# Kernel optimization log

Hardware: AMD Instinct MI355X
Metric: run time of the kernel (lower is better)

## Reference

```python
import jax, jax.numpy as jnp
import numpy as np

N = 100000   # nodes
E = 3200000  # edges (avg degree 32)
F = 128      # input node feature dim
C = 32       # GCSConv channels
H = 24       # dense1 units


def setup_inputs() -> dict:
    key = jax.random.key(0)
    ks = jax.random.split(key, 12)
    rng = np.random.default_rng(0)
    src = rng.integers(0, N, size=E, dtype=np.int32)
    dst = rng.integers(0, N, size=E, dtype=np.int32)
    # GCN-style symmetric normalization weights: D^{-1/2} A D^{-1/2}
    deg_out = np.maximum(np.bincount(src, minlength=N), 1).astype(np.float32)
    deg_in = np.maximum(np.bincount(dst, minlength=N), 1).astype(np.float32)
    w = 1.0 / np.sqrt(deg_out[src] * deg_in[dst])
    glorot = lambda k, fin, fout: jax.random.normal(k, (fin, fout), jnp.float32) * np.sqrt(2.0 / (fin + fout))
    return {
        "x": jax.random.normal(ks[0], (N, F), jnp.float32),
        "edge_src": jnp.asarray(src),
        "edge_dst": jnp.asarray(dst),
        "edge_w": jnp.asarray(w),
        "K1a": glorot(ks[1], F, C), "K2a": glorot(ks[2], F, C), "ba": jnp.zeros((C,), jnp.float32),
        "K1b": glorot(ks[3], C, C), "K2b": glorot(ks[4], C, C), "bb": jnp.zeros((C,), jnp.float32),
        "Wd1": glorot(ks[5], C, H), "bd1": jnp.zeros((H,), jnp.float32),
        "Wd2": glorot(ks[6], H, 1), "bd2": jnp.zeros((1,), jnp.float32),
    }


def _gcs_conv(x, src, dst, w, K1, K2, b):
    # Spektral GCSConv: relu(A_norm @ (x @ K1) + x @ K2 + b)
    h = x @ K1                                   # [N, C] transform first (cheap dim)
    msg = h[src] * w[:, None]                    # [E, C] gather + scale
    agg = jax.ops.segment_sum(msg, dst, num_segments=N)  # [N, C] scatter-add
    return jax.nn.relu(agg + x @ K2 + b)


def reference(x, edge_src, edge_dst, edge_w, K1a, K2a, ba, K1b, K2b, bb, Wd1, bd1, Wd2, bd2):
    x = _gcs_conv(x, edge_src, edge_dst, edge_w, K1a, K2a, ba)
    x = _gcs_conv(x, edge_src, edge_dst, edge_w, K1b, K2b, bb)
    pooled = jnp.sum(x, axis=0, keepdims=True)   # GlobalSumPool -> [1, C]
    out = pooled @ Wd1 + bd1                     # Dense(24), linear
    out = out @ Wd2 + bd2                        # Dense(1), linear
    return out
```

## Files before the change

kernel.cpp:

```cpp
#include <hip/hip_runtime.h>
#include <hip/hip_bf16.h>

typedef unsigned long long ull;
typedef unsigned int uint;
typedef unsigned short ushort;

using bf16x8 = __attribute__((ext_vector_type(8))) short;
using f32x4  = __attribute__((ext_vector_type(4))) float;


#define CHUNK    8192
#define NPB      256
#define NBMAX    512
#define STAGECAP 9216

__device__ __forceinline__ ushort f2bf(float f) {
    __hip_bfloat16 b = __float2bfloat16(f);
    return *reinterpret_cast<ushort*>(&b);
}
__device__ __forceinline__ uint pack2(float a, float b) {
    return (uint)f2bf(a) | ((uint)f2bf(b) << 16);
}
__device__ __forceinline__ void bf16x4_decode(uint2 hv, float& f0, float& f1,
                                              float& f2, float& f3) {
    f0 = __uint_as_float(hv.x << 16);
    f1 = __uint_as_float(hv.x & 0xFFFF0000u);
    f2 = __uint_as_float(hv.y << 16);
    f3 = __uint_as_float(hv.y & 0xFFFF0000u);
}

__global__ __launch_bounds__(256) void prep_weights(
    const float* __restrict__ K1a, const float* __restrict__ K2a,
    const float* __restrict__ K1b, const float* __restrict__ K2b,
    ushort* __restrict__ Kca, ushort* __restrict__ Kcb)
{
    int t = blockIdx.x * 256 + threadIdx.x;
    if (t < 8192) {
        int col = t >> 7, k = t & 127;
        float v = (col < 32) ? K1a[k * 32 + col] : K2a[k * 32 + col - 32];
        Kca[col * 128 + k] = f2bf(v);
    }
    if (t < 2048) {
        int col = t >> 5, k = t & 31;
        float v = (col < 32) ? K1b[k * 32 + col] : K2b[k * 32 + col - 32];
        Kcb[col * 32 + k] = f2bf(v);
    }
}

__global__ __launch_bounds__(512) void build_runs_kernel(
    const int* __restrict__ src, const int* __restrict__ dst,
    const float* __restrict__ w,
    ull* __restrict__ etmp, int* __restrict__ runoff,
    int* __restrict__ bucket_cnt, int e, int nruns, int nb)
{
    __shared__ ull stage[CHUNK];
    __shared__ int hist[NBMAX];
    __shared__ int scn[NBMAX];
    const int r = blockIdx.x, tid = threadIdx.x;
    const int base = r * CHUNK;
    const int cnt = min(CHUNK, e - base);

    hist[tid] = 0;
    __syncthreads();

    int dreg[CHUNK / 512];
    #pragma unroll
    for (int k = 0; k < CHUNK / 512; ++k) {
        int i = tid + k * 512;
        int d = (i < cnt) ? dst[base + i] : -1;
        dreg[k] = d;
        if (d >= 0) atomicAdd(&hist[d >> 8], 1);
    }
    __syncthreads();

    int v = hist[tid];
    scn[tid] = v;
    __syncthreads();
    for (int off = 1; off < NBMAX; off <<= 1) {
        int u = (tid >= off) ? scn[tid - off] : 0;
        __syncthreads();
        scn[tid] += u;
        __syncthreads();
    }
    const int ex = scn[tid] - v;
    if (tid < nb && v) atomicAdd(&bucket_cnt[tid], v);
    hist[tid] = ex;
    if (tid <= nb) runoff[(size_t)r * (nb + 1) + tid] = base + ex;
    __syncthreads();

    #pragma unroll
    for (int k = 0; k < CHUNK / 512; ++k) {
        int i = tid + k * 512;
        int d = dreg[k];
        if (d >= 0) {
            int pos = atomicAdd(&hist[d >> 8], 1);
            unsigned lo = (unsigned)src[base + i] | ((unsigned)(d & 255) << 20);
            stage[pos] = (ull)lo | ((ull)__float_as_uint(w[base + i]) << 32);
        }
    }
    __syncthreads();

    for (int i = tid; i < cnt; i += 512) etmp[base + i] = stage[i];
}

__global__ __launch_bounds__(512) void bucket_scan_kernel(
    const int* __restrict__ cnt, int* __restrict__ basep, int nb, int e)
{
    __shared__ int s[512];
    int t = threadIdx.x;
    int v = (t < nb) ? cnt[t] : 0;
    s[t] = v; __syncthreads();
    for (int off = 1; off < 512; off <<= 1) {
        int u = (t >= off) ? s[t - off] : 0;
        __syncthreads(); s[t] += u; __syncthreads();
    }
    if (t < nb) basep[t] = s[t] - v;
    if (t == 0) basep[nb] = e;
}

__global__ __launch_bounds__(512) void sort_buckets_kernel(
    const ull* __restrict__ etmp, const int* __restrict__ runoff,
    const int* __restrict__ bbase,
    ull* __restrict__ epack, int* __restrict__ row,
    int n, int e, int nruns, int nb)
{
    __shared__ ull stage[STAGECAP];
    __shared__ int hist[NPB];
    __shared__ int scn[NPB];
    __shared__ int cur[NPB];
    const int b = blockIdx.x, tid = threadIdx.x;
    const int base0 = bbase[b];
    const int cnt = bbase[b + 1] - base0;

    if (tid < NPB) hist[tid] = 0;
    __syncthreads();

    const int stream = tid >> 3, sub = tid & 7;
    const int* rs = runoff;

    for (int r = stream; r < nruns; r += 64) {
        int s0 = rs[(size_t)r * (nb + 1) + b];
        int s1 = rs[(size_t)r * (nb + 1) + b + 1];
        for (int i = s0 + sub; i < s1; i += 8)
            atomicAdd(&hist[(int)((etmp[i] >> 20) & 255u)], 1);
    }
    __syncthreads();

    int v = (tid < NPB) ? hist[tid] : 0;
    if (tid < NPB) scn[tid] = v;
    __syncthreads();
    for (int off = 1; off < NPB; off <<= 1) {
        int u = (tid >= off && tid < NPB) ? scn[tid - off] : 0;
        __syncthreads();
        if (tid < NPB) scn[tid] += u;
        __syncthreads();
    }
    if (tid < NPB) {
        int ex = scn[tid] - v;
        cur[tid] = ex;
        int node = b * NPB + tid;
        if (node < n) row[node] = base0 + ex;
    }
    if (b == nb - 1 && tid == 0) row[n] = e;
    __syncthreads();

    if (cnt <= STAGECAP) {
        for (int r = stream; r < nruns; r += 64) {
            int s0 = rs[(size_t)r * (nb + 1) + b];
            int s1 = rs[(size_t)r * (nb + 1) + b + 1];
            for (int i = s0 + sub; i < s1; i += 8) {
                ull pk = etmp[i];
                int pos = atomicAdd(&cur[(int)((pk >> 20) & 255u)], 1);
                stage[pos] = pk;
            }
        }
        __syncthreads();
        for (int i = tid; i < cnt; i += 512) epack[(size_t)base0 + i] = stage[i];
    } else {
        for (int r = stream; r < nruns; r += 64) {
            int s0 = rs[(size_t)r * (nb + 1) + b];
            int s1 = rs[(size_t)r * (nb + 1) + b + 1];
            for (int i = s0 + sub; i < s1; i += 8) {
                ull pk = etmp[i];
                int pos = atomicAdd(&cur[(int)((pk >> 20) & 255u)], 1);
                epack[(size_t)base0 + pos] = pk;
            }
        }
    }
}

__global__ __launch_bounds__(256) void gemm_mfma_a(
    const float* __restrict__ x, const ushort* __restrict__ Kca,
    const float* __restrict__ bias,
    ushort* __restrict__ h, float* __restrict__ p, int n)
{
    __shared__ ushort xs[64 * 136];
    const int tid = threadIdx.x;
    const int base = blockIdx.x * 64;

    for (int idx = tid; idx < 64 * 16; idx += 256) {
        int nl = idx >> 4, c8 = idx & 15;
        int node = base + nl;
        float4 v0 = make_float4(0.f, 0.f, 0.f, 0.f);
        float4 v1 = v0;
        if (node < n) {
            const float* xp = x + (size_t)node * 128 + c8 * 8;
            v0 = *(const float4*)xp;
            v1 = *(const float4*)(xp + 4);
        }
        uint4 u;
        u.x = pack2(v0.x, v0.y); u.y = pack2(v0.z, v0.w);
        u.z = pack2(v1.x, v1.y); u.w = pack2(v1.z, v1.w);
        *(uint4*)&xs[nl * 136 + c8 * 8] = u;
    }
    __syncthreads();

    const int lane = tid & 63, w = tid >> 6;
    const int r15 = lane & 15, g = lane >> 4;
    const int nbase = w * 16;

    f32x4 acc[4] = {{0.f,0.f,0.f,0.f},{0.f,0.f,0.f,0.f},
                    {0.f,0.f,0.f,0.f},{0.f,0.f,0.f,0.f}};

    #pragma unroll
    for (int kk = 0; kk < 4; ++kk) {
        bf16x8 af = *(const bf16x8*)&xs[(nbase + r15) * 136 + kk * 32 + g * 8];
        #pragma unroll
        for (int t = 0; t < 4; ++t) {
            bf16x8 bfr = *(const bf16x8*)&Kca[(size_t)(t * 16 + r15) * 128 + kk * 32 + g * 8];
            acc[t] = __builtin_amdgcn_mfma_f32_16x16x32_bf16(af, bfr, acc[t], 0, 0, 0);
        }
    }

    #pragma unroll
    for (int t = 0; t < 4; ++t) {
        int col = t * 16 + r15;
        float bv = (col >= 32) ? bias[col - 32] : 0.f;
        #pragma unroll
        for (int i = 0; i < 4; ++i) {
            int node = base + nbase + g * 4 + i;
            if (node < n) {
                float v = acc[t][i];
                if (col < 32) h[(size_t)node * 32 + col] = f2bf(v);
                else          p[(size_t)node * 32 + col - 32] = v + bv;
            }
        }
    }
}

__global__ __launch_bounds__(256) void gemm_mfma_b(
    const ushort* __restrict__ x1, const ushort* __restrict__ Kcb,
    const float* __restrict__ bias,
    ushort* __restrict__ h, float* __restrict__ p, int n)
{
    __shared__ ushort xs[64 * 40];
    const int tid = threadIdx.x;
    const int base = blockIdx.x * 64;

    {
        int nl = tid >> 2, c8 = tid & 3;
        int node = base + nl;
        uint4 u = make_uint4(0u, 0u, 0u, 0u);
        if (node < n) u = *(const uint4*)(x1 + (size_t)node * 32 + c8 * 8);
        *(uint4*)&xs[nl * 40 + c8 * 8] = u;
    }
    __syncthreads();

    const int lane = tid & 63, w = tid >> 6;
    const int r15 = lane & 15, g = lane >> 4;
    const int nbase = w * 16;

    f32x4 acc[4] = {{0.f,0.f,0.f,0.f},{0.f,0.f,0.f,0.f},
                    {0.f,0.f,0.f,0.f},{0.f,0.f,0.f,0.f}};

    bf16x8 af = *(const bf16x8*)&xs[(nbase + r15) * 40 + g * 8];
    #pragma unroll
    for (int t = 0; t < 4; ++t) {
        bf16x8 bfr = *(const bf16x8*)&Kcb[(size_t)(t * 16 + r15) * 32 + g * 8];
        acc[t] = __builtin_amdgcn_mfma_f32_16x16x32_bf16(af, bfr, acc[t], 0, 0, 0);
    }

    #pragma unroll
    for (int t = 0; t < 4; ++t) {
        int col = t * 16 + r15;
        float bv = (col >= 32) ? bias[col - 32] : 0.f;
        #pragma unroll
        for (int i = 0; i < 4; ++i) {
            int node = base + nbase + g * 4 + i;
            if (node < n) {
                float v = acc[t][i];
                if (col < 32) h[(size_t)node * 32 + col] = f2bf(v);
                else          p[(size_t)node * 32 + col - 32] = v + bv;
            }
        }
    }
}

__device__ __forceinline__ float4 gather_node(
    const int* __restrict__ row, const ull* __restrict__ epack,
    const ushort* __restrict__ h, int node, int q)
{
    int r0 = row[node], r1 = row[node + 1];
    float4 a = make_float4(0.f, 0.f, 0.f, 0.f);
    float4 b = make_float4(0.f, 0.f, 0.f, 0.f);
    int i = r0;
    for (; i + 7 < r1; i += 8) {
        ull pk[8];
        uint2 hv[8];
        #pragma unroll
        for (int u = 0; u < 8; ++u) pk[u] = epack[i + u];
        #pragma unroll
        for (int u = 0; u < 8; ++u)
            hv[u] = *(const uint2*)(h + (size_t)(pk[u] & 0xFFFFFu) * 32 + q * 4);
        #pragma unroll
        for (int u = 0; u < 8; ++u) {
            float wv = __uint_as_float((uint)(pk[u] >> 32));
            float f0, f1, f2, f3;
            bf16x4_decode(hv[u], f0, f1, f2, f3);
            if (u & 1) {
                b.x = fmaf(wv, f0, b.x); b.y = fmaf(wv, f1, b.y);
                b.z = fmaf(wv, f2, b.z); b.w = fmaf(wv, f3, b.w);
            } else {
                a.x = fmaf(wv, f0, a.x); a.y = fmaf(wv, f1, a.y);
                a.z = fmaf(wv, f2, a.z); a.w = fmaf(wv, f3, a.w);
            }
        }
    }
    for (; i + 3 < r1; i += 4) {
        ull pk[4];
        uint2 hv[4];
        #pragma unroll
        for (int u = 0; u < 4; ++u) pk[u] = epack[i + u];
        #pragma unroll
        for (int u = 0; u < 4; ++u)
            hv[u] = *(const uint2*)(h + (size_t)(pk[u] & 0xFFFFFu) * 32 + q * 4);
        #pragma unroll
        for (int u = 0; u < 4; ++u) {
            float wv = __uint_as_float((uint)(pk[u] >> 32));
            float f0, f1, f2, f3;
            bf16x4_decode(hv[u], f0, f1, f2, f3);
            if (u & 1) {
                b.x = fmaf(wv, f0, b.x); b.y = fmaf(wv, f1, b.y);
                b.z = fmaf(wv, f2, b.z); b.w = fmaf(wv, f3, b.w);
            } else {
                a.x = fmaf(wv, f0, a.x); a.y = fmaf(wv, f1, a.y);
                a.z = fmaf(wv, f2, a.z); a.w = fmaf(wv, f3, a.w);
            }
        }
    }
    for (; i < r1; ++i) {
        ull p0 = epack[i];
        uint2 h0 = *(const uint2*)(h + (size_t)(p0 & 0xFFFFFu) * 32 + q * 4);
        float w0 = __uint_as_float((uint)(p0 >> 32));
        float f0, f1, f2, f3;
        bf16x4_decode(h0, f0, f1, f2, f3);
        a.x = fmaf(w0, f0, a.x); a.y = fmaf(w0, f1, a.y);
        a.z = fmaf(w0, f2, a.z); a.w = fmaf(w0, f3, a.w);
    }
    a.x += b.x; a.y += b.y; a.z += b.z; a.w += b.w;
    return a;
}

__global__ __launch_bounds__(256) void gather_x1_kernel(
    const int* __restrict__ row, const ull* __restrict__ epack,
    const ushort* __restrict__ h, const float* __restrict__ p,
    ushort* __restrict__ x1, int n)
{
    const int q = threadIdx.x & 7;
    const int node = blockIdx.x * 32 + (threadIdx.x >> 3);
    if (node >= n) return;
    float4 acc = gather_node(row, epack, h, node, q);
    const float4 pv = *(const float4*)(p + (size_t)node * 32 + q * 4);
    float4 o;
    o.x = fmaxf(acc.x + pv.x, 0.f);
    o.y = fmaxf(acc.y + pv.y, 0.f);
    o.z = fmaxf(acc.z + pv.z, 0.f);
    o.w = fmaxf(acc.w + pv.w, 0.f);
    uint2 u;
    u.x = pack2(o.x, o.y);
    u.y = pack2(o.z, o.w);
    *(uint2*)(x1 + (size_t)node * 32 + q * 4) = u;
}

__global__ __launch_bounds__(256) void gather_pool_kernel(
    const int* __restrict__ row, const ull* __restrict__ epack,
    const ushort* __restrict__ h, const float* __restrict__ p,
    float* __restrict__ pooled, int n)
{
    const int q = threadIdx.x & 7;
    const int node = blockIdx.x * 32 + (threadIdx.x >> 3);

    float4 o = make_float4(0.f, 0.f, 0.f, 0.f);
    if (node < n) {
        float4 acc = gather_node(row, epack, h, node, q);
        const float4 pv = *(const float4*)(p + (size_t)node * 32 + q * 4);
        o.x = fmaxf(acc.x + pv.x, 0.f);
        o.y = fmaxf(acc.y + pv.y, 0.f);
        o.z = fmaxf(acc.z + pv.z, 0.f);
        o.w = fmaxf(acc.w + pv.w, 0.f);
    }
    __shared__ float red[256][4];
    red[threadIdx.x][0] = o.x; red[threadIdx.x][1] = o.y;
    red[threadIdx.x][2] = o.z; red[threadIdx.x][3] = o.w;
    __syncthreads();
    if (threadIdx.x < 32) {
        const int c = threadIdx.x;
        const int cq = c >> 2, cj = c & 3;
        float s = 0.f;
        #pragma unroll
        for (int l = 0; l < 32; ++l) s += red[l * 8 + cq][cj];
        unsafeAtomicAdd(&pooled[c], s);
    }
}

__device__ __forceinline__ void store_row_bf16(ushort* out, const float* acc) {
    uint u[16];
    #pragma unroll
    for (int k = 0; k < 16; ++k) u[k] = pack2(acc[2 * k], acc[2 * k + 1]);
    uint4* o = (uint4*)out;
    o[0] = make_uint4(u[0], u[1], u[2], u[3]);
    o[1] = make_uint4(u[4], u[5], u[6], u[7]);
    o[2] = make_uint4(u[8], u[9], u[10], u[11]);
    o[3] = make_uint4(u[12], u[13], u[14], u[15]);
}

__global__ __launch_bounds__(128) void gemm_f32_a(
    const float* __restrict__ x, const float* __restrict__ K1,
    const float* __restrict__ K2, const float* __restrict__ bias,
    ushort* __restrict__ h, float* __restrict__ p, int n)
{
    __shared__ float xs[64 * 129];
    const int base = blockIdx.x * 64;
    for (int i = threadIdx.x; i < 64 * 32; i += 128) {
        int r = i >> 5, c4 = i & 31;
        int node = base + r;
        float4 v = make_float4(0.f, 0.f, 0.f, 0.f);
        if (node < n) v = *(const float4*)(x + (size_t)node * 128 + c4 * 4);
        float* d = &xs[r * 129 + c4 * 4];
        d[0] = v.x; d[1] = v.y; d[2] = v.z; d[3] = v.w;
    }
    __syncthreads();
    const int nl = threadIdx.x & 63;
    const int node = base + nl;
    if (node >= n) return;
    float acc[32];
    #pragma unroll
    for (int c = 0; c < 32; ++c) acc[c] = 0.f;
    const float* xr = &xs[nl * 129];
    const float* K = (threadIdx.x < 64) ? K1 : K2;
    for (int k = 0; k < 128; ++k) {
        float xv = xr[k];
        #pragma unroll
        for (int c = 0; c < 32; ++c) acc[c] = fmaf(xv, K[k * 32 + c], acc[c]);
    }
    if (threadIdx.x < 64) {
        store_row_bf16(h + (size_t)node * 32, acc);
    } else {
        #pragma unroll
        for (int c = 0; c < 32; ++c) acc[c] += bias[c];
        float* out = p + (size_t)node * 32;
        #pragma unroll
        for (int c4 = 0; c4 < 8; ++c4)
            *(float4*)(out + c4 * 4) = make_float4(acc[c4*4], acc[c4*4+1], acc[c4*4+2], acc[c4*4+3]);
    }
}

__global__ __launch_bounds__(128) void gemm_f32_b(
    const float* __restrict__ x1,
    const float* __restrict__ K1, const float* __restrict__ K2,
    const float* __restrict__ bias,
    ushort* __restrict__ h, float* __restrict__ p, int n)
{
    __shared__ float xs[64 * 33];
    const int base = blockIdx.x * 64;
    for (int i = threadIdx.x; i < 64 * 8; i += 128) {
        int r = i >> 3, c4 = i & 7;
        int node = base + r;
        float4 a = make_float4(0.f, 0.f, 0.f, 0.f);
        if (node < n) a = *(const float4*)(x1 + (size_t)node * 32 + c4 * 4);
        float* d = &xs[r * 33 + c4 * 4];
        d[0] = a.x; d[1] = a.y; d[2] = a.z; d[3] = a.w;
    }
    __syncthreads();
    const int nl = threadIdx.x & 63;
    const int node = base + nl;
    if (node >= n) return;
    float acc[32];
    #pragma unroll
    for (int c = 0; c < 32; ++c) acc[c] = 0.f;
    const float* xr = &xs[nl * 33];
    const float* K = (threadIdx.x < 64) ? K1 : K2;
    for (int k = 0; k < 32; ++k) {
        float xv = xr[k];
        #pragma unroll
        for (int c = 0; c < 32; ++c) acc[c] = fmaf(xv, K[k * 32 + c], acc[c]);
    }
    if (threadIdx.x < 64) {
        store_row_bf16(h + (size_t)node * 32, acc);
    } else {
        #pragma unroll
        for (int c = 0; c < 32; ++c) acc[c] += bias[c];
        float* out = p + (size_t)node * 32;
        #pragma unroll
        for (int c4 = 0; c4 < 8; ++c4)
            *(float4*)(out + c4 * 4) = make_float4(acc[c4*4], acc[c4*4+1], acc[c4*4+2], acc[c4*4+3]);
    }
}

__global__ __launch_bounds__(256) void edge_scatter(
    const int* __restrict__ src, const int* __restrict__ dst,
    const float* __restrict__ w, const ushort* __restrict__ h,
    float* __restrict__ agg, int e)
{
    int t = blockIdx.x * 256 + threadIdx.x;
    int eid = t >> 3, q = t & 7;
    if (eid >= e) return;
    int s = src[eid];
    int d = dst[eid];
    float wv = w[eid];
    uint2 hv = *(const uint2*)(h + (size_t)s * 32 + q * 4);
    float f0, f1, f2, f3;
    bf16x4_decode(hv, f0, f1, f2, f3);
    float* ap = agg + (size_t)d * 32 + q * 4;
    unsafeAtomicAdd(ap + 0, f0 * wv);
    unsafeAtomicAdd(ap + 1, f1 * wv);
    unsafeAtomicAdd(ap + 2, f2 * wv);
    unsafeAtomicAdd(ap + 3, f3 * wv);
}

__global__ __launch_bounds__(256) void relu_add_kernel(
    const float* __restrict__ a, const float* __restrict__ b,
    float* __restrict__ o, size_t m)
{
    size_t i = (size_t)blockIdx.x * 256 + threadIdx.x;
    if (i < m) o[i] = fmaxf(a[i] + b[i], 0.f);
}

__global__ __launch_bounds__(256) void pool_kernel(
    const float* __restrict__ p, const float* __restrict__ agg,
    float* __restrict__ pooled, int n)
{
    const int ch = threadIdx.x & 31;
    const int r  = threadIdx.x >> 5;
    float acc = 0.f;
    for (int node = blockIdx.x * 8 + r; node < n; node += gridDim.x * 8) {
        size_t idx = (size_t)node * 32 + ch;
        acc += fmaxf(p[idx] + agg[idx], 0.f);
    }
    __shared__ float red[256];
    red[threadIdx.x] = acc;
    __syncthreads();
    if (threadIdx.x < 32) {
        float s = 0.f;
        #pragma unroll
        for (int i = 0; i < 8; ++i) s += red[i * 32 + ch];
        unsafeAtomicAdd(&pooled[ch], s);
    }
}

__global__ void dense_kernel(
    const float* __restrict__ pooled,
    const float* __restrict__ Wd1, const float* __restrict__ bd1,
    const float* __restrict__ Wd2, const float* __restrict__ bd2,
    float* __restrict__ out)
{
    int j = threadIdx.x;
    float t = 0.f;
    if (j < 24) {
        t = bd1[j];
        #pragma unroll
        for (int c = 0; c < 32; ++c) t = fmaf(pooled[c], Wd1[c * 24 + j], t);
        t *= Wd2[j];
    }
    #pragma unroll
    for (int off = 32; off > 0; off >>= 1) t += __shfl_down(t, off, 64);
    if (j == 0) out[0] = t + bd2[0];
}

extern "C" void kernel_launch(void* const* d_in, const int* in_sizes, int n_in,
                              void* d_out, int out_size, void* d_ws, size_t ws_size,
                              hipStream_t stream) {
    const float* x   = (const float*)d_in[0];
    const int*   esrc= (const int*)d_in[1];
    const int*   edst= (const int*)d_in[2];
    const float* ew  = (const float*)d_in[3];
    const float* K1a = (const float*)d_in[4];
    const float* K2a = (const float*)d_in[5];
    const float* ba  = (const float*)d_in[6];
    const float* K1b = (const float*)d_in[7];
    const float* K2b = (const float*)d_in[8];
    const float* bb  = (const float*)d_in[9];
    const float* Wd1 = (const float*)d_in[10];
    const float* bd1 = (const float*)d_in[11];
    const float* Wd2 = (const float*)d_in[12];
    const float* bd2 = (const float*)d_in[13];

    const int n = in_sizes[0] / 128;
    const int e = in_sizes[1];
    const size_t nc = (size_t)n * 32;
    const int nb = (n + NPB - 1) / NPB;
    const int nruns = (e + CHUNK - 1) / CHUNK;

    const size_t ab_bytes = nc * 2 + nc * 4;
    const size_t etmp_bytes = ((size_t)e * 8 > ab_bytes) ? (size_t)e * 8 : ab_bytes;
    const size_t need = (size_t)e * 8 + etmp_bytes + nc * 4 + 32 * 4
                      + (size_t)(n + 1) * 4 + (size_t)nb * 4 + (size_t)(nb + 1) * 4
                      + (size_t)nruns * (nb + 1) * 4
                      + (8192 + 2048) * 2 + 256;

    const int gemm_blocks   = (n + 63) / 64;
    const int gather_blocks = (n + 31) / 32;

    if (ws_size >= need && nb <= NBMAX) {
        char* wp = (char*)d_ws;
        ull* epack = (ull*)wp;                wp += (size_t)e * 8;
        ull* etmp  = (ull*)wp;
        ushort* A = (ushort*)etmp;
        float* B = (float*)(A + nc);          wp += etmp_bytes;
        ushort* x1b = (ushort*)wp;            wp += nc * 4;
        float* pooled = (float*)wp;           wp += 32 * 4;
        int* row = (int*)wp;                  wp += (size_t)(n + 1) * 4;
        int* bucket_cnt = (int*)wp;           wp += (size_t)nb * 4;
        int* bucket_base = (int*)wp;          wp += (size_t)(nb + 1) * 4;
        int* runoff = (int*)wp;               wp += (size_t)nruns * (nb + 1) * 4;
        ushort* Kca = (ushort*)wp;            wp += 8192 * 2;
        ushort* Kcb = (ushort*)wp;

        hipMemsetAsync(bucket_cnt, 0, (size_t)nb * 4, stream);
        hipMemsetAsync(pooled, 0, 32 * 4, stream);

        prep_weights<<<32, 256, 0, stream>>>(K1a, K2a, K1b, K2b, Kca, Kcb);
        build_runs_kernel<<<nruns, 512, 0, stream>>>(esrc, edst, ew, etmp, runoff,
                                                     bucket_cnt, e, nruns, nb);
        bucket_scan_kernel<<<1, 512, 0, stream>>>(bucket_cnt, bucket_base, nb, e);
        sort_buckets_kernel<<<nb, 512, 0, stream>>>(etmp, runoff, bucket_base,
                                                    epack, row, n, e, nruns, nb);
        gemm_mfma_a<<<gemm_blocks, 256, 0, stream>>>(x, Kca, ba, A, B, n);
        gather_x1_kernel<<<gather_blocks, 256, 0, stream>>>(row, epack, A, B, x1b, n);
        gemm_mfma_b<<<gemm_blocks, 256, 0, stream>>>(x1b, Kcb, bb, A, B, n);
        gather_pool_kernel<<<gather_blocks, 256, 0, stream>>>(row, epack, A, B, pooled, n);
        dense_kernel<<<1, 64, 0, stream>>>(pooled, Wd1, bd1, Wd2, bd2, (float*)d_out);
    } else {
        ushort* A     = (ushort*)d_ws;
        float* B      = (float*)(A + 2 * nc);
        float* Cg     = B + nc;
        float* pooled = Cg + nc;
        const int edge_blocks_8 = (int)(((long long)e * 8 + 255) / 256);

        hipMemsetAsync(Cg, 0, nc * 4, stream);
        gemm_f32_a<<<gemm_blocks, 128, 0, stream>>>(x, K1a, K2a, ba, A, B, n);
        edge_scatter<<<edge_blocks_8, 256, 0, stream>>>(esrc, edst, ew, A, Cg, e);
        relu_add_kernel<<<(int)((nc + 255) / 256), 256, 0, stream>>>(B, Cg, B, nc);
        gemm_f32_b<<<gemm_blocks, 128, 0, stream>>>(B, K1b, K2b, bb, A, Cg, n);
        hipMemsetAsync(B, 0, nc * 4, stream);
        edge_scatter<<<edge_blocks_8, 256, 0, stream>>>(esrc, edst, ew, A, B, e);
        hipMemsetAsync(pooled, 0, 32 * 4, stream);
        pool_kernel<<<1024, 256, 0, stream>>>(Cg, B, pooled, n);
        dense_kernel<<<1, 64, 0, stream>>>(pooled, Wd1, bd1, Wd2, bd2, (float*)d_out);
    }
}
```

Baseline: 217.6 us.

## Split gather feature table into column halves and store skip term in bf16

The h table is written as two separate 16-column bf16 planes, and each gather kernel runs twice, once per half. Each pass's random-access working set is half the size, so it should fit better in cache. The skip/bias term p is also stored in bf16 instead of fp32, and the edge stream and row loads use nontemporal hints so they do not evict h. The cost is reading the edge list twice per layer and some precision loss in p.

```diff
diff --git a/kernel.cpp b/kernel.cpp
--- a/kernel.cpp
+++ b/kernel.cpp
@@ -27,6 +27,9 @@
     f1 = __uint_as_float(hv.x & 0xFFFF0000u);
     f2 = __uint_as_float(hv.y << 16);
     f3 = __uint_as_float(hv.y & 0xFFFF0000u);
+}
+__device__ __forceinline__ uint2 u2_of_ull(ull v) {
+    uint2 u; u.x = (uint)v; u.y = (uint)(v >> 32); return u;
 }
 
 __global__ __launch_bounds__(256) void prep_weights(
@@ -192,11 +195,12 @@
 __global__ __launch_bounds__(256) void gemm_mfma_a(
     const float* __restrict__ x, const ushort* __restrict__ Kca,
     const float* __restrict__ bias,
-    ushort* __restrict__ h, float* __restrict__ p, int n)
+    ushort* __restrict__ h, ushort* __restrict__ p, int n)
 {
     __shared__ ushort xs[64 * 136];
     const int tid = threadIdx.x;
     const int base = blockIdx.x * 64;
+    const size_t nc16 = (size_t)n * 16;
 
     for (int idx = tid; idx < 64 * 16; idx += 256) {
         int nl = idx >> 4, c8 = idx & 15;
@@ -234,15 +238,17 @@
 
     #pragma unroll
     for (int t = 0; t < 4; ++t) {
-        int col = t * 16 + r15;
-        float bv = (col >= 32) ? bias[col - 32] : 0.f;
         #pragma unroll
         for (int i = 0; i < 4; ++i) {
             int node = base + nbase + g * 4 + i;
             if (node < n) {
                 float v = acc[t][i];
-                if (col < 32) h[(size_t)node * 32 + col] = f2bf(v);
-                else          p[(size_t)node * 32 + col - 32] = v + bv;
+                if (t < 2) {
+                    h[(size_t)t * nc16 + (size_t)node * 16 + r15] = f2bf(v);
+                } else {
+                    int pcol = (t - 2) * 16 + r15;
+                    p[(size_t)node * 32 + pcol] = f2bf(v + bias[pcol]);
+                }
             }
         }
     }
@@ -251,11 +257,12 @@
 __global__ __launch_bounds__(256) void gemm_mfma_b(
     const ushort* __restrict__ x1, const ushort* __restrict__ Kcb,
     const float* __restrict__ bias,
-    ushort* __restrict__ h, float* __restrict__ p, int n)
+    ushort* __restrict__ h, ushort* __restrict__ p, int n)
 {
     __shared__ ushort xs[64 * 40];
     const int tid = threadIdx.x;
     const int base = blockIdx.x * 64;
+    const size_t nc16 = (size_t)n * 16;
 
     {
         int nl = tid >> 2, c8 = tid & 3;
@@ -282,25 +289,28 @@
 
     #pragma unroll
     for (int t = 0; t < 4; ++t) {
-        int col = t * 16 + r15;
-        float bv = (col >= 32) ? bias[col - 32] : 0.f;
         #pragma unroll
         for (int i = 0; i < 4; ++i) {
             int node = base + nbase + g * 4 + i;
             if (node < n) {
                 float v = acc[t][i];
-                if (col < 32) h[(size_t)node * 32 + col] = f2bf(v);
-                else          p[(size_t)node * 32 + col - 32] = v + bv;
+                if (t < 2) {
+                    h[(size_t)t * nc16 + (size_t)node * 16 + r15] = f2bf(v);
+                } else {
+                    int pcol = (t - 2) * 16 + r15;
+                    p[(size_t)node * 32 + pcol] = f2bf(v + bias[pcol]);
+                }
             }
         }
     }
 }
 
-__device__ __forceinline__ float4 gather_node(
+__device__ __forceinline__ float4 gather_node_half(
     const int* __restrict__ row, const ull* __restrict__ epack,
-    const ushort* __restrict__ h, int node, int q)
-{
-    int r0 = row[node], r1 = row[node + 1];
+    const ushort* __restrict__ hTab, int node, int q)
+{
+    int r0 = __builtin_nontemporal_load(&row[node]);
+    int r1 = __builtin_nontemporal_load(&row[node + 1]);
     float4 a = make_float4(0.f, 0.f, 0.f, 0.f);
     float4 b = make_float4(0.f, 0.f, 0.f, 0.f);
     int i = r0;
@@ -308,10 +318,10 @@
         ull pk[8];
         uint2 hv[8];
         #pragma unroll
-        for (int u = 0; u < 8; ++u) pk[u] = epack[i + u];
+        for (int u = 0; u < 8; ++u) pk[u] = __builtin_nontemporal_load(&epack[i + u]);
         #pragma unroll
         for (int u = 0; u < 8; ++u)
-            hv[u] = *(const uint2*)(h + (size_t)(pk[u] & 0xFFFFFu) * 32 + q * 4);
+            hv[u] = *(const uint2*)(hTab + (size_t)(pk[u] & 0xFFFFFu) * 16 + q * 4);
         #pragma unroll
         for (int u = 0; u < 8; ++u) {
             float wv = __uint_as_float((uint)(pk[u] >> 32));
@@ -330,10 +340,10 @@
         ull pk[4];
         uint2 hv[4];
         #pragma unroll
-        for (int u = 0; u < 4; ++u) pk[u] = epack[i + u];
+        for (int u = 0; u < 4; ++u) pk[u] = __builtin_nontemporal_load(&epack[i + u]);
         #pragma unroll
         for (int u = 0; u < 4; ++u)
-            hv[u] = *(const uint2*)(h + (size_t)(pk[u] & 0xFFFFFu) * 32 + q * 4);
+            hv[u] = *(const uint2*)(hTab + (size_t)(pk[u] & 0xFFFFFu) * 16 + q * 4);
         #pragma unroll
         for (int u = 0; u < 4; ++u) {
             float wv = __uint_as_float((uint)(pk[u] >> 32));
@@ -349,8 +359,8 @@
         }
     }
     for (; i < r1; ++i) {
-        ull p0 = epack[i];
-        uint2 h0 = *(const uint2*)(h + (size_t)(p0 & 0xFFFFFu) * 32 + q * 4);
+        ull p0 = __builtin_nontemporal_load(&epack[i]);
+        uint2 h0 = *(const uint2*)(hTab + (size_t)(p0 & 0xFFFFFu) * 16 + q * 4);
         float w0 = __uint_as_float((uint)(p0 >> 32));
         float f0, f1, f2, f3;
         bf16x4_decode(h0, f0, f1, f2, f3);
@@ -361,55 +371,58 @@
     return a;
 }
 
-__global__ __launch_bounds__(256) void gather_x1_kernel(
+__global__ __launch_bounds__(256) void gather_x1_half(
     const int* __restrict__ row, const ull* __restrict__ epack,
-    const ushort* __restrict__ h, const float* __restrict__ p,
-    ushort* __restrict__ x1, int n)
-{
-    const int q = threadIdx.x & 7;
-    const int node = blockIdx.x * 32 + (threadIdx.x >> 3);
+    const ushort* __restrict__ hTab, const ushort* __restrict__ p,
+    ushort* __restrict__ x1, int n, int halfOff)
+{
+    const int q = threadIdx.x & 3;
+    const int node = blockIdx.x * 64 + (threadIdx.x >> 2);
     if (node >= n) return;
-    float4 acc = gather_node(row, epack, h, node, q);
-    const float4 pv = *(const float4*)(p + (size_t)node * 32 + q * 4);
-    float4 o;
-    o.x = fmaxf(acc.x + pv.x, 0.f);
-    o.y = fmaxf(acc.y + pv.y, 0.f);
-    o.z = fmaxf(acc.z + pv.z, 0.f);
-    o.w = fmaxf(acc.w + pv.w, 0.f);
-    uint2 u;
-    u.x = pack2(o.x, o.y);
-    u.y = pack2(o.z, o.w);
-    *(uint2*)(x1 + (size_t)node * 32 + q * 4) = u;
-}
-
-__global__ __launch_bounds__(256) void gather_pool_kernel(
+    float4 acc = gather_node_half(row, epack, hTab, node, q);
+    ull praw = __builtin_nontemporal_load(
+        (const ull*)(p + (size_t)node * 32 + halfOff + q * 4));
+    float f0, f1, f2, f3;
+    bf16x4_decode(u2_of_ull(praw), f0, f1, f2, f3);
+    float o0 = fmaxf(acc.x + f0, 0.f);
+    float o1 = fmaxf(acc.y + f1, 0.f);
+    float o2 = fmaxf(acc.z + f2, 0.f);
+    float o3 = fmaxf(acc.w + f3, 0.f);
+    ull ov = (ull)pack2(o0, o1) | ((ull)pack2(o2, o3) << 32);
+    __builtin_nontemporal_store(ov, (ull*)(x1 + (size_t)node * 32 + halfOff + q * 4));
+}
+
+__global__ __launch_bounds__(256) void gather_pool_half(
     const int* __restrict__ row, const ull* __restrict__ epack,
-    const ushort* __restrict__ h, const float* __restrict__ p,
-    float* __restrict__ pooled, int n)
-{
-    const int q = threadIdx.x & 7;
-    const int node = blockIdx.x * 32 + (threadIdx.x >> 3);
+    const ushort* __restrict__ hTab, const ushort* __restrict__ p,
+    float* __restrict__ pooled, int n, int halfOff)
+{
+    const int q = threadIdx.x & 3;
+    const int node = blockIdx.x * 64 + (threadIdx.x >> 2);
 
     float4 o = make_float4(0.f, 0.f, 0.f, 0.f);
     if (node < n) {
-        float4 acc = gather_node(row, epack, h, node, q);
-        const float4 pv = *(const float4*)(p + (size_t)node * 32 + q * 4);
-        o.x = fmaxf(acc.x + pv.x, 0.f);
-        o.y = fmaxf(acc.y + pv.y, 0.f);
-        o.z = fmaxf(acc.z + pv.z, 0.f);
-        o.w = fmaxf(acc.w + pv.w, 0.f);
+        float4 acc = gather_node_half(row, epack, hTab, node, q);
+        ull praw = __builtin_nontemporal_load(
+            (const ull*)(p + (size_t)node * 32 + halfOff + q * 4));
+        float f0, f1, f2, f3;
+        bf16x4_decode(u2_of_ull(praw), f0, f1, f2, f3);
+        o.x = fmaxf(acc.x + f0, 0.f);
+        o.y = fmaxf(acc.y + f1, 0.f);
+        o.z = fmaxf(acc.z + f2, 0.f);
+        o.w = fmaxf(acc.w + f3, 0.f);
     }
     __shared__ float red[256][4];
     red[threadIdx.x][0] = o.x; red[threadIdx.x][1] = o.y;
     red[threadIdx.x][2] = o.z; red[threadIdx.x][3] = o.w;
     __syncthreads();
-    if (threadIdx.x < 32) {
+    if (threadIdx.x < 16) {
         const int c = threadIdx.x;
         const int cq = c >> 2, cj = c & 3;
         float s = 0.f;
         #pragma unroll
-        for (int l = 0; l < 32; ++l) s += red[l * 8 + cq][cj];
-        unsafeAtomicAdd(&pooled[c], s);
+        for (int g = 0; g < 64; ++g) s += red[g * 4 + cq][cj];
+        unsafeAtomicAdd(&pooled[halfOff + c], s);
     }
 }
 
@@ -598,10 +611,11 @@
     const int n = in_sizes[0] / 128;
     const int e = in_sizes[1];
     const size_t nc = (size_t)n * 32;
+    const size_t nc16 = (size_t)n * 16;
     const int nb = (n + NPB - 1) / NPB;
     const int nruns = (e + CHUNK - 1) / CHUNK;
 
-    const size_t ab_bytes = nc * 2 + nc * 4;
+    const size_t ab_bytes = nc * 2 + nc * 2;
     const size_t etmp_bytes = ((size_t)e * 8 > ab_bytes) ? (size_t)e * 8 : ab_bytes;
     const size_t need = (size_t)e * 8 + etmp_bytes + nc * 4 + 32 * 4
                       + (size_t)(n + 1) * 4 + (size_t)nb * 4 + (size_t)(nb + 1) * 4
@@ -609,14 +623,15 @@
                       + (8192 + 2048) * 2 + 256;
 
     const int gemm_blocks   = (n + 63) / 64;
-    const int gather_blocks = (n + 31) / 32;
+    const int gather_blocks = (n + 63) / 64;
 
     if (ws_size >= need && nb <= NBMAX) {
         char* wp = (char*)d_ws;
         ull* epack = (ull*)wp;                wp += (size_t)e * 8;
         ull* etmp  = (ull*)wp;
-        ushort* A = (ushort*)etmp;
-        float* B = (float*)(A + nc);          wp += etmp_bytes;
+        ushort* A  = (ushort*)etmp;
+        ushort* Bp = A + nc;
+        wp += etmp_bytes;
         ushort* x1b = (ushort*)wp;            wp += nc * 4;
         float* pooled = (float*)wp;           wp += 32 * 4;
         int* row = (int*)wp;                  wp += (size_t)(n + 1) * 4;
@@ -635,10 +650,12 @@
         bucket_scan_kernel<<<1, 512, 0, stream>>>(bucket_cnt, bucket_base, nb, e);
         sort_buckets_kernel<<<nb, 512, 0, stream>>>(etmp, runoff, bucket_base,
                                                     epack, row, n, e, nruns, nb);
-        gemm_mfma_a<<<gemm_blocks, 256, 0, stream>>>(x, Kca, ba, A, B, n);
-        gather_x1_kernel<<<gather_blocks, 256, 0, stream>>>(row, epack, A, B, x1b, n);
-        gemm_mfma_b<<<gemm_blocks, 256, 0, stream>>>(x1b, Kcb, bb, A, B, n);
-        gather_pool_kernel<<<gather_blocks, 256, 0, stream>>>(row, epack, A, B, pooled, n);
+        gemm_mfma_a<<<gemm_blocks, 256, 0, stream>>>(x, Kca, ba, A, Bp, n);
+        gather_x1_half<<<gather_blocks, 256, 0, stream>>>(row, epack, A, Bp, x1b, n, 0);
+        gather_x1_half<<<gather_blocks, 256, 0, stream>>>(row, epack, A + nc16, Bp, x1b, n, 16);
+        gemm_mfma_b<<<gemm_blocks, 256, 0, stream>>>(x1b, Kcb, bb, A, Bp, n);
+        gather_pool_half<<<gather_blocks, 256, 0, stream>>>(row, epack, A, Bp, pooled, n, 0);
+        gather_pool_half<<<gather_blocks, 256, 0, stream>>>(row, epack, A + nc16, Bp, pooled, n, 16);
         dense_kernel<<<1, 64, 0, stream>>>(pooled, Wd1, bd1, Wd2, bd2, (float*)d_out);
     } else {
         ushort* A     = (ushort*)d_ws;
```

Result: slower. 302.6 us (+39.1%).
